# Kernel tuning notes

Hardware: AMD Instinct MI355X
Metric: run time of the kernel (lower is better)

Reference implementation:

```python
import jax, jax.numpy as jnp
import numpy as np

NEARZERO = 1e-5
# parameter bounds in dict order: BETA, FC, K0, K1, K2, LP, PERC, UZL, TT, CFMAX, CFR, CWH
BOUNDS = np.array([[1.0, 6.0], [50.0, 1000.0], [0.05, 0.9], [0.01, 0.5],
                   [0.001, 0.2], [0.2, 1.0], [0.0, 10.0], [0.0, 100.0],
                   [-2.5, 2.5], [0.5, 10.0], [0.0, 0.1], [0.0, 0.2]],
                  dtype=np.float32)


def setup_inputs() -> dict:
    key = jax.random.key(0)
    k1, k2 = jax.random.split(key)
    Nstep, Ngrid, nmul = 730, 10000, 1
    x = jax.random.uniform(k1, (Nstep, Ngrid, 3), dtype=jnp.float32)
    parameters = jax.random.uniform(k2, (Nstep, Ngrid, 12, nmul), dtype=jnp.float32)
    return {"x": x, "parameters": parameters}


def _hbv_forward(x, parameters):
    # static params taken at static_idx = warm_up - 1 = -1 (last timestep)
    lo = jnp.asarray(BOUNDS[:, 0])[None, :, None]
    hi = jnp.asarray(BOUNDS[:, 1])[None, :, None]
    ps = lo + parameters[-1] * (hi - lo)          # [Ngrid, 12, nmul]
    BETA, FC, K0, K1, K2, LP, PERCmax, UZL, TT, CFMAX, CFR, CWH = (
        ps[:, i, :] for i in range(12))           # each [Ngrid, nmul]

    # forcings, broadcast over nmul via trailing singleton dim
    P = x[:, :, 0:1]    # [Nstep, Ngrid, 1]
    T = x[:, :, 1:2]
    PET = x[:, :, 2:3]

    state0 = tuple(jnp.full(FC.shape, 0.001, jnp.float32) for _ in range(5))

    def step(carry, inp):
        SNOWPACK, MELTWATER, SM, SUZ, SLZ = carry
        Pt, Tt, PETt = inp                        # [Ngrid, 1] each
        is_rain = (Tt >= TT).astype(jnp.float32)
        RAIN = Pt * is_rain
        SNOW = Pt * (1.0 - is_rain)
        SNOWPACK = SNOWPACK + SNOW
        melt = jnp.minimum(jnp.maximum(CFMAX * (Tt - TT), 0.0), SNOWPACK)
        MELTWATER = MELTWATER + melt
        SNOWPACK = SNOWPACK - melt
        refreezing = jnp.minimum(jnp.maximum(CFR * CFMAX * (TT - Tt), 0.0), MELTWATER)
        SNOWPACK = SNOWPACK + refreezing
        MELTWATER = MELTWATER - refreezing
        tosoil = jnp.maximum(MELTWATER - CWH * SNOWPACK, 0.0)
        MELTWATER = MELTWATER - tosoil
        soil_wetness = jnp.clip((SM / FC) ** BETA, 0.0, 1.0)
        recharge = (RAIN + tosoil) * soil_wetness
        SM = SM + RAIN + tosoil - recharge
        excess = jnp.maximum(SM - FC, 0.0)
        evapfactor = jnp.clip(SM / (LP * FC), 0.0, 1.0)
        ETact = jnp.minimum(SM, PETt * evapfactor)
        SM = jnp.maximum(SM - ETact, NEARZERO)
        SUZ = SUZ + recharge + excess
        PERC = jnp.minimum(SUZ, PERCmax)
        SUZ = SUZ - PERC
        Q0 = K0 * jnp.maximum(SUZ - UZL, 0.0)
        SUZ = SUZ - Q0
        Q1 = K1 * SUZ
        SUZ = SUZ - Q1
        SLZ = SLZ + PERC
        Q2 = K2 * SLZ
        SLZ = SLZ - Q2
        Qsim = Q0 + Q1 + Q2
        return (SNOWPACK, MELTWATER, SM, SUZ, SLZ), (Qsim, ETact, SNOWPACK)

    _, (Qsimmu, AET, SWE) = jax.lax.scan(step, state0, (P, T, PET))
    # routing=False path: Qs = mean over nmul, unsqueezed
    flow_sim = Qsimmu.mean(-1, keepdims=True)     # [Nstep, Ngrid, 1]
    AET_hydro = AET.mean(-1, keepdims=True)
    SWE_out = SWE.mean(-1, keepdims=True)
    return flow_sim, AET_hydro, SWE_out


def reference(x, parameters):
    return _hbv_forward(x, parameters)
```

## Files before the change

kernel.cpp:

```cpp
#include <hip/hip_runtime.h>

#define NSTEP 730
#define NGRID 10000
#define DPF 10

__global__ __launch_bounds__(64) void hbv_kernel(
    const float* __restrict__ x, const float* __restrict__ params,
    float* __restrict__ out)
{
    const int g = blockIdx.x * 64 + threadIdx.x;
    if (g >= NGRID) return;

    const long pbase = ((long)(NSTEP - 1) * NGRID + g) * 12;
    float pr[12];
#pragma unroll
    for (int i = 0; i < 12; ++i) pr[i] = params[pbase + i];

    const float lo[12] = {1.0f, 50.0f, 0.05f, 0.01f, 0.001f, 0.2f, 0.0f, 0.0f, -2.5f, 0.5f, 0.0f, 0.0f};
    const float hi[12] = {6.0f, 1000.0f, 0.9f, 0.5f, 0.2f, 1.0f, 10.0f, 100.0f, 2.5f, 10.0f, 0.1f, 0.2f};
    float ps[12];
#pragma unroll
    for (int i = 0; i < 12; ++i) ps[i] = lo[i] + pr[i] * (hi[i] - lo[i]);

    const float BETA = ps[0], FC = ps[1], K0 = ps[2], K1 = ps[3], K2 = ps[4], LP = ps[5],
                PERCmax = ps[6], UZL = ps[7], TT = ps[8], CFMAX = ps[9], CFR = ps[10], CWH = ps[11];

    const float rFC = 1.0f / FC;
    const float rLPFC = 1.0f / (LP * FC);
    const float CFRxCFMAX = CFR * CFMAX;

    float SNOWPACK = 0.001f, MELTWATER = 0.001f, SM = 0.001f, SUZ = 0.001f, SLZ = 0.001f;

    const float* xg = x + (long)g * 3;
    const long stepStride = (long)NGRID * 3;
    float* outQ = out + g;
    float* outE = out + (long)NSTEP * NGRID + g;
    float* outS = out + 2L * NSTEP * NGRID + g;

    float bP[DPF], bT[DPF], bE[DPF];
#pragma unroll
    for (int d = 0; d < DPF; ++d) {
        const float* p = xg + (long)d * stepStride;
        bP[d] = p[0]; bT[d] = p[1]; bE[d] = p[2];
    }

    for (int t0 = 0; t0 < NSTEP; t0 += DPF) {
        float nP[DPF], nT[DPF], nE[DPF];
#pragma unroll
        for (int d = 0; d < DPF; ++d) {
            int tt = t0 + DPF + d;
            if (tt > NSTEP - 1) tt = NSTEP - 1;
            const float* p = xg + (long)tt * stepStride;
            nP[d] = p[0]; nT[d] = p[1]; nE[d] = p[2];
        }

#pragma unroll
        for (int d = 0; d < DPF; ++d) {
            const float Pt = bP[d], Tt = bT[d], PETt = bE[d];

            const float RAIN = (Tt >= TT) ? Pt : 0.0f;
            const float SNOW = Pt - RAIN;
            SNOWPACK += SNOW;
            const float melt = fminf(fmaxf(CFMAX * (Tt - TT), 0.0f), SNOWPACK);
            MELTWATER += melt;
            SNOWPACK -= melt;
            const float refreeze = fminf(fmaxf(CFRxCFMAX * (TT - Tt), 0.0f), MELTWATER);
            SNOWPACK += refreeze;
            MELTWATER -= refreeze;
            const float tosoil = fmaxf(MELTWATER - CWH * SNOWPACK, 0.0f);
            MELTWATER -= tosoil;

            const float ratio = SM * rFC;
            float sw = __builtin_amdgcn_exp2f(BETA * __builtin_amdgcn_logf(ratio));
            sw = fminf(fmaxf(sw, 0.0f), 1.0f);
            const float rt = RAIN + tosoil;
            const float recharge = rt * sw;
            SM = SM + rt - recharge;
            const float excess = fmaxf(SM - FC, 0.0f);
            const float evapf = fminf(fmaxf(SM * rLPFC, 0.0f), 1.0f);
            const float ETact = fminf(SM, PETt * evapf);
            SM = fmaxf(SM - ETact, 1e-5f);

            SUZ = SUZ + recharge + excess;
            const float PERC = fminf(SUZ, PERCmax);
            SUZ -= PERC;
            const float Q0 = K0 * fmaxf(SUZ - UZL, 0.0f);
            SUZ -= Q0;
            const float Q1 = K1 * SUZ;
            SUZ -= Q1;
            SLZ += PERC;
            const float Q2 = K2 * SLZ;
            SLZ -= Q2;

            const long o = (long)(t0 + d) * NGRID;
            outQ[o] = Q0 + Q1 + Q2;
            outE[o] = ETact;
            outS[o] = SNOWPACK;
        }

#pragma unroll
        for (int d = 0; d < DPF; ++d) { bP[d] = nP[d]; bT[d] = nT[d]; bE[d] = nE[d]; }
    }
}

extern "C" void kernel_launch(void* const* d_in, const int* in_sizes, int n_in,
                              void* d_out, int out_size, void* d_ws, size_t ws_size,
                              hipStream_t stream) {
    const float* x = (const float*)d_in[0];
    const float* params = (const float*)d_in[1];
    float* out = (float*)d_out;
    const int threads = 64;
    const int blocks = (NGRID + threads - 1) / threads;
    hbv_kernel<<<blocks, threads, 0, stream>>>(x, params, out);
}
```

Before: 535.4 us.

## Double-buffer forcing prefetch with ping-pong chunks and 32-bit offsets

Replaces the copy-based prefetch buffer with two alternating register buffers (A/B ping-pong), so the next chunk of forcings loads while the current chunk computes and no register copies are needed. Address math moves to 32-bit unsigned offsets with running increments, and the step math is simplified: shared melt/refreeze product, some redundant clamps dropped, and bucket updates rewritten as (1-K) multiplies. Adds launch_bounds(64,1), which allows more registers per thread. The removed clamps and reordered arithmetic may change rounding slightly.

```diff
diff --git a/kernel.cpp b/kernel.cpp
--- a/kernel.cpp
+++ b/kernel.cpp
@@ -4,14 +4,14 @@
 #define NGRID 10000
 #define DPF 10
 
-__global__ __launch_bounds__(64) void hbv_kernel(
+__global__ __launch_bounds__(64, 1) void hbv_kernel(
     const float* __restrict__ x, const float* __restrict__ params,
     float* __restrict__ out)
 {
     const int g = blockIdx.x * 64 + threadIdx.x;
     if (g >= NGRID) return;
 
-    const long pbase = ((long)(NSTEP - 1) * NGRID + g) * 12;
+    const unsigned pbase = (unsigned)((NSTEP - 1) * NGRID + g) * 12u;
     float pr[12];
 #pragma unroll
     for (int i = 0; i < 12; ++i) pr[i] = params[pbase + i];
@@ -25,82 +25,91 @@
     const float BETA = ps[0], FC = ps[1], K0 = ps[2], K1 = ps[3], K2 = ps[4], LP = ps[5],
                 PERCmax = ps[6], UZL = ps[7], TT = ps[8], CFMAX = ps[9], CFR = ps[10], CWH = ps[11];
 
-    const float rFC = 1.0f / FC;
+    const float rFC   = 1.0f / FC;
     const float rLPFC = 1.0f / (LP * FC);
-    const float CFRxCFMAX = CFR * CFMAX;
+    const float nCFR  = -CFR;
+    const float omK1  = 1.0f - K1;
+    const float omK2  = 1.0f - K2;
 
     float SNOWPACK = 0.001f, MELTWATER = 0.001f, SM = 0.001f, SUZ = 0.001f, SLZ = 0.001f;
 
-    const float* xg = x + (long)g * 3;
-    const long stepStride = (long)NGRID * 3;
-    float* outQ = out + g;
-    float* outE = out + (long)NSTEP * NGRID + g;
-    float* outS = out + 2L * NSTEP * NGRID + g;
+    float* __restrict__ const outQ = out;
+    float* __restrict__ const outE = out + (unsigned)(NSTEP * NGRID);
+    float* __restrict__ const outS = out + 2u * (unsigned)(NSTEP * NGRID);
 
+    unsigned pfOff = (unsigned)g * 3u;
+    unsigned stOff = (unsigned)g;
+
+#define PF(P_, T_, E_) do {                                                  \
+    _Pragma("unroll")                                                        \
+    for (int d = 0; d < DPF; ++d) {                                          \
+        const unsigned o_ = pfOff + (unsigned)(d * 3 * NGRID);               \
+        P_[d] = x[o_]; T_[d] = x[o_ + 1u]; E_[d] = x[o_ + 2u];               \
+    }                                                                        \
+    pfOff += (unsigned)(DPF * 3 * NGRID);                                    \
+} while (0)
+
+#define CHUNK(P_, T_, E_) do {                                               \
+    _Pragma("unroll")                                                        \
+    for (int d = 0; d < DPF; ++d) {                                          \
+        const float Pt = P_[d], Tt = T_[d], PETt = E_[d];                    \
+        const float dT   = Tt - TT;                                          \
+        const float RAIN = (dT >= 0.0f) ? Pt : 0.0f;                         \
+        SNOWPACK += Pt - RAIN;                                               \
+        const float m0   = CFMAX * dT;                                       \
+        const float melt = fminf(fmaxf(m0, 0.0f), SNOWPACK);                 \
+        MELTWATER += melt;                                                   \
+        SNOWPACK  -= melt;                                                   \
+        const float refreeze = fminf(fmaxf(nCFR * m0, 0.0f), MELTWATER);     \
+        SNOWPACK  += refreeze;                                               \
+        MELTWATER -= refreeze;                                               \
+        const float tosoil = fmaxf(MELTWATER - CWH * SNOWPACK, 0.0f);        \
+        MELTWATER -= tosoil;                                                 \
+         \
+         \
+        const float sw = fminf(                                              \
+            __builtin_amdgcn_exp2f(BETA * __builtin_amdgcn_logf(SM * rFC)),  \
+            1.0f);                                                           \
+        const float rt       = RAIN + tosoil;                                \
+        const float recharge = rt * sw;                                      \
+        SM += rt - recharge;                                                 \
+        const float excess = fmaxf(SM - FC, 0.0f);                           \
+        const float evapf  = fminf(SM * rLPFC, 1.0f);  \
+        const float ETact  = fminf(SM, PETt * evapf);                        \
+        SM = fmaxf(SM - ETact, 1e-5f);                                       \
+        SUZ += recharge + excess;                                            \
+        const float PERC = fminf(SUZ, PERCmax);                              \
+        SUZ -= PERC;                                                         \
+        const float Q0   = K0 * fmaxf(SUZ - UZL, 0.0f);                      \
+        const float suz1 = SUZ - Q0;                                         \
+        const float Q1   = K1 * suz1;                                        \
+        SUZ = omK1 * suz1;               \
+        const float t2 = SLZ + PERC;                                         \
+        const float Q2 = K2 * t2;                                            \
+        SLZ = omK2 * t2;                 \
+        outQ[stOff] = (Q0 + Q1) + Q2;                                        \
+        outE[stOff] = ETact;                                                 \
+        outS[stOff] = SNOWPACK;                                              \
+        stOff += (unsigned)NGRID;                                            \
+    }                                                                        \
+} while (0)
+
+    float aP[DPF], aT[DPF], aE[DPF];
     float bP[DPF], bT[DPF], bE[DPF];
-#pragma unroll
-    for (int d = 0; d < DPF; ++d) {
-        const float* p = xg + (long)d * stepStride;
-        bP[d] = p[0]; bT[d] = p[1]; bE[d] = p[2];
+
+    PF(aP, aT, aE);
+
+#pragma unroll 1
+    for (int c = 0; c < 72; c += 2) {
+        PF(bP, bT, bE);
+        CHUNK(aP, aT, aE);
+        PF(aP, aT, aE);
+        CHUNK(bP, bT, bE);
     }
+    CHUNK(aP, aT, aE);
 
-    for (int t0 = 0; t0 < NSTEP; t0 += DPF) {
-        float nP[DPF], nT[DPF], nE[DPF];
-#pragma unroll
-        for (int d = 0; d < DPF; ++d) {
-            int tt = t0 + DPF + d;
-            if (tt > NSTEP - 1) tt = NSTEP - 1;
-            const float* p = xg + (long)tt * stepStride;
-            nP[d] = p[0]; nT[d] = p[1]; nE[d] = p[2];
-        }
-
-#pragma unroll
-        for (int d = 0; d < DPF; ++d) {
-            const float Pt = bP[d], Tt = bT[d], PETt = bE[d];
-
-            const float RAIN = (Tt >= TT) ? Pt : 0.0f;
-            const float SNOW = Pt - RAIN;
-            SNOWPACK += SNOW;
-            const float melt = fminf(fmaxf(CFMAX * (Tt - TT), 0.0f), SNOWPACK);
-            MELTWATER += melt;
-            SNOWPACK -= melt;
-            const float refreeze = fminf(fmaxf(CFRxCFMAX * (TT - Tt), 0.0f), MELTWATER);
-            SNOWPACK += refreeze;
-            MELTWATER -= refreeze;
-            const float tosoil = fmaxf(MELTWATER - CWH * SNOWPACK, 0.0f);
-            MELTWATER -= tosoil;
-
-            const float ratio = SM * rFC;
-            float sw = __builtin_amdgcn_exp2f(BETA * __builtin_amdgcn_logf(ratio));
-            sw = fminf(fmaxf(sw, 0.0f), 1.0f);
-            const float rt = RAIN + tosoil;
-            const float recharge = rt * sw;
-            SM = SM + rt - recharge;
-            const float excess = fmaxf(SM - FC, 0.0f);
-            const float evapf = fminf(fmaxf(SM * rLPFC, 0.0f), 1.0f);
-            const float ETact = fminf(SM, PETt * evapf);
-            SM = fmaxf(SM - ETact, 1e-5f);
-
-            SUZ = SUZ + recharge + excess;
-            const float PERC = fminf(SUZ, PERCmax);
-            SUZ -= PERC;
-            const float Q0 = K0 * fmaxf(SUZ - UZL, 0.0f);
-            SUZ -= Q0;
-            const float Q1 = K1 * SUZ;
-            SUZ -= Q1;
-            SLZ += PERC;
-            const float Q2 = K2 * SLZ;
-            SLZ -= Q2;
-
-            const long o = (long)(t0 + d) * NGRID;
-            outQ[o] = Q0 + Q1 + Q2;
-            outE[o] = ETact;
-            outS[o] = SNOWPACK;
-        }
-
-#pragma unroll
-        for (int d = 0; d < DPF; ++d) { bP[d] = nP[d]; bT[d] = nT[d]; bE[d] = nE[d]; }
-    }
+#undef PF
+#undef CHUNK
 }
 
 extern "C" void kernel_launch(void* const* d_in, const int* in_sizes, int n_in,
```

New measurement: 525.9 us. Within noise of the previous version (-1.8%).
